# Performance work log

Measured on AMD Instinct MI355X. Metric: run time of the kernel, lower is better.

## Reference

```python
import jax, jax.numpy as jnp
import numpy as np

NB_STEPS = 50
ALPHA = 0.9
NUM_RNN_STEPS = 2
B = 4096
NUM_FEATURE = 100
IN_D = 5
HIDDEN = [64, 64, 64]
P1 = (1.1, 1.1, 1.5, 2.0, 2.5)   # IntegrandNN_outer_level powers
P2 = (1.5, 2.0, 2.5, 3.0, 3.5)   # IntegrandNN powers


def _cc(nb_steps):
    # Clenshaw-Curtis weights/steps, identical to UMNN's compute_cc_weights
    n = nb_steps
    i = np.arange(n + 1, dtype=np.float64).reshape(-1, 1)
    lam = np.cos(i @ i.T * np.pi / n)
    lam[:, 0] = 0.5
    lam[:, -1] *= 0.5
    lam = lam * 2.0 / n
    W = np.zeros(n + 1)
    even = np.arange(0, n + 1, 2)
    W[even] = 2.0 / (1.0 - even.astype(np.float64) ** 2)
    W[0] = 1.0
    ccw = (lam.T @ W).astype(np.float32)                         # [n+1]
    steps = np.cos(np.arange(n + 1) * np.pi / n).astype(np.float32)  # [n+1]
    return jnp.asarray(ccw), jnp.asarray(steps)

CC_W, CC_S = _cc(NB_STEPS)


def _mlp(xh, Ws, bs):
    # Linear+ReLU stack with ELU on the last layer (ReLU popped, ELU appended)
    h = xh
    for W, b in zip(Ws[:-1], bs[:-1]):
        h = jax.nn.relu(h @ W.T + b)
    return jax.nn.elu(h @ Ws[-1].T + bs[-1])


def _integrand(x, h, Ws, bs, Wf, powers):
    z = _mlp(jnp.concatenate([x, h], axis=1), Ws, bs) + 1.0      # [N,1], z >= 0
    feats = jnp.concatenate([z ** p for p in powers], axis=1)    # [N,5]
    return jax.nn.relu((1.0 / (feats + 1.0)) @ Wf.T)             # [N,1]


def _integrate(x0, xT, h, f):
    # ParallelNeuralIntegral forward: CC quadrature of f from x0 to xT
    Bn, S = x0.shape[0], NB_STEPS + 1
    X = x0[:, None, :] + (xT - x0)[:, None, :] * (CC_S[None, :, None] + 1.0) / 2.0  # [B,S,1]
    hs = jnp.broadcast_to(h[:, None, :], (Bn, S, h.shape[1])).reshape(-1, h.shape[1])
    dz = f(X.reshape(-1, 1), hs).reshape(Bn, S, 1)
    return (dz * CC_W[None, :, None]).sum(1) * (xT - x0) / 2.0   # [B,1]


def setup_inputs() -> dict:
    key = jax.random.key(0)
    ks = jax.random.split(key, 24)
    def lin(k, o, i):
        return jax.random.normal(k, (o, i), jnp.float32) / np.sqrt(i)
    d = {}
    d["x_"] = jax.random.normal(ks[0], (B, NUM_FEATURE), jnp.float32)
    d["h_"] = jax.random.normal(ks[1], (B, IN_D - 1), jnp.float32)
    d["log_weight"] = jnp.ones((1, NUM_FEATURE), jnp.float32)     # reset_parameters -> 1
    d["sigmoid_param"] = jnp.zeros((1,), jnp.float32)
    sizes = [IN_D] + HIDDEN + [1]
    for tag, base in (("f1", 2), ("f2", 12)):
        for li, (i, o) in enumerate(zip(sizes[:-1], sizes[1:])):
            d[f"{tag}_W{li}"] = lin(ks[base + 2 * li], o, i)
            d[f"{tag}_b{li}"] = jnp.zeros((o,), jnp.float32)
        d[f"{tag}_Wf"] = jnp.abs(lin(ks[base + 9], 1, 5))         # reset_params -> abs
    return d


def reference(x_, h_, log_weight, sigmoid_param,
              f1_W0, f1_b0, f1_W1, f1_b1, f1_W2, f1_b2, f1_W3, f1_b3, f1_Wf,
              f2_W0, f2_b0, f2_W1, f2_b1, f2_W2, f2_b2, f2_W3, f2_b3, f2_Wf):
    f1Ws = [f1_W0, f1_W1, f1_W2, f1_W3]; f1bs = [f1_b0, f1_b1, f1_b2, f1_b3]
    f2Ws = [f2_W0, f2_W1, f2_W2, f2_W3]; f2bs = [f2_b0, f2_b1, f2_b2, f2_b3]
    f1 = lambda x, h: _integrand(x, h, f1Ws, f1bs, f1_Wf, P1)
    f2 = lambda x, h: _integrand(x, h, f2Ws, f2bs, f2_Wf, P2)

    # modular function: linear to [B,1] then sum over dim 1 -> [B,1]
    xm = jnp.sum(x_ * log_weight[0], axis=1, keepdims=True)
    lam = jax.nn.sigmoid(sigmoid_param[0])

    I1 = jnp.zeros_like(xm)
    I2 = jnp.zeros_like(xm)
    out_first = None
    for _ in range(NUM_RNN_STEPS):
        x = (1.0 - lam) * xm + lam * I1
        x2 = (1.0 - lam) * xm + lam * I2
        out_first = f1(x2, h_)
        I1 = _integrate(jnp.zeros_like(x), x, h_, f1)
        xmax = jnp.max(x2) + 10.0
        xfinal = jnp.zeros_like(x) + xmax
        I2 = (1.0 / ALPHA) * _integrate(x2, xfinal, h_, f2)
    return I1, out_first, I2
```

## Files before the change

kernel.cpp:

```cpp
#include <hip/hip_runtime.h>
#include <math.h>

typedef _Float16 half8v __attribute__((ext_vector_type(8)));
typedef _Float16 half4v __attribute__((ext_vector_type(4)));
typedef _Float16 half2v __attribute__((ext_vector_type(2)));
typedef float float4v __attribute__((ext_vector_type(4)));

#define BB    4096
#define INV_ALPHA (1.0f/0.9f)

#define WS_CCW  0
#define WS_CCS  64
#define WS_LAM  128
#define WS_PM   256
#define WS_XM   512
#define WS_A1   4608
#define WS_A2   8704
#define WS_H    16384
#define H_NET   8192
#define H_W2    4096
#define H_W0    16384
#define H_W3    20480

#if defined(__has_builtin)
#if __has_builtin(__builtin_amdgcn_rcpf)
#define FRCP(x) __builtin_amdgcn_rcpf(x)
#endif
#if __has_builtin(__builtin_amdgcn_exp2f)
#define FEXP2(x) __builtin_amdgcn_exp2f(x)
#endif
#if __has_builtin(__builtin_amdgcn_logf)
#define FLOG2(x) __builtin_amdgcn_logf(x)
#endif
#endif
#ifndef FRCP
#define FRCP(x) (1.0f / (x))
#endif
#ifndef FEXP2
#define FEXP2(x) exp2f(x)
#endif
#ifndef FLOG2
#define FLOG2(x) log2f(x)
#endif

__device__ __forceinline__ int swz(int row, int cb) {
    return (row << 6) + (((cb ^ (row & 7)) & 7) << 3);
}

__device__ __forceinline__ half4v pk_relu4(float4v c) {
#if defined(__has_builtin) && __has_builtin(__builtin_amdgcn_cvt_pkrtz)
    half2v a = __builtin_bit_cast(half2v,
        __builtin_amdgcn_cvt_pkrtz(fmaxf(c[0], 0.0f), fmaxf(c[1], 0.0f)));
    half2v b = __builtin_bit_cast(half2v,
        __builtin_amdgcn_cvt_pkrtz(fmaxf(c[2], 0.0f), fmaxf(c[3], 0.0f)));
    half4v o; o[0] = a[0]; o[1] = a[1]; o[2] = b[0]; o[3] = b[1];
    return o;
#else
    half4v o;
    o[0] = (_Float16)fmaxf(c[0], 0.0f); o[1] = (_Float16)fmaxf(c[1], 0.0f);
    o[2] = (_Float16)fmaxf(c[2], 0.0f); o[3] = (_Float16)fmaxf(c[3], 0.0f);
    return o;
#endif
}

__device__ __forceinline__ float tail5(float y,
        float p0, float p1, float p2, float p3, float p4,
        float wf0, float wf1, float wf2, float wf3, float wf4) {
    if (y <= 0.0f) y = FEXP2(y * 1.44269504f) - 1.0f;
    float z = y + 1.0f;
    float lg = FLOG2(z);
    float g = wf0 * FRCP(FEXP2(p0 * lg) + 1.0f)
            + wf1 * FRCP(FEXP2(p1 * lg) + 1.0f)
            + wf2 * FRCP(FEXP2(p2 * lg) + 1.0f)
            + wf3 * FRCP(FEXP2(p3 * lg) + 1.0f)
            + wf4 * FRCP(FEXP2(p4 * lg) + 1.0f);
    return fmaxf(g, 0.0f);
}

__global__ void k_setup(const float* __restrict__ x_, const float* __restrict__ lw,
                        const float* __restrict__ sp,
                        const float* __restrict__ f1W0, const float* __restrict__ f1W1,
                        const float* __restrict__ f1W2, const float* __restrict__ f1W3,
                        const float* __restrict__ f2W0, const float* __restrict__ f2W1,
                        const float* __restrict__ f2W2, const float* __restrict__ f2W3,
                        float* __restrict__ ws, float* __restrict__ out) {
    _Float16* wh = (_Float16*)(ws + WS_H);
    const int blk = blockIdx.x, tid = threadIdx.x;
    if (blk < 256) {
        int wave = tid >> 6, lane = tid & 63;
        float vmax = -1e30f;
        for (int r = 0; r < 4; ++r) {
            int row = blk * 16 + wave * 4 + r;
            float v = 0.0f;
            for (int i = lane; i < 100; i += 64) v = fmaf(x_[row * 100 + i], lw[i], v);
            #pragma unroll
            for (int off = 32; off > 0; off >>= 1) v += __shfl_xor(v, off, 64);
            if (lane == 0) ws[WS_XM + row] = v;
            vmax = fmaxf(vmax, v);
        }
        __shared__ float sm[4];
        if (lane == 0) sm[wave] = vmax;
        __syncthreads();
        if (tid == 0)
            ws[WS_PM + blk] = fmaxf(fmaxf(sm[0], sm[1]), fmaxf(sm[2], sm[3]));
    } else if (blk < 272) {
        int t = (blk - 256) * 256 + tid;
        wh[t]                = (_Float16)f1W1[t];
        wh[H_W2 + t]         = (_Float16)f1W2[t];
        wh[H_NET + t]        = (_Float16)f2W1[t];
        wh[H_NET + H_W2 + t] = (_Float16)f2W2[t];
        if (t < 2048) {
            int j = t >> 5, k = t & 31;
            wh[H_W0 + t]        = (k < 5) ? (_Float16)f1W0[j * 5 + k] : (_Float16)0.0f;
            wh[H_W0 + 2048 + t] = (k < 5) ? (_Float16)f2W0[j * 5 + k] : (_Float16)0.0f;
        }
        if (t < 64) {
            wh[H_W3 + t]      = (_Float16)f1W3[t];
            wh[H_W3 + 64 + t] = (_Float16)f2W3[t];
        }
    } else if (blk == 272) {
        if (tid == 64) ws[WS_LAM] = 1.0f / (1.0f + expf(-sp[0]));
        if (tid <= 50) {
            int s = tid;
            ws[WS_CCS + s] = cospif((float)s / 50.0f);
            float acc = 0.0f;
            for (int a = 0; a <= 50; ++a) {
                float w;
                if (a == 0) w = 1.0f;
                else if ((a & 1) == 0) w = 2.0f / (1.0f - (float)(a * a));
                else continue;
                float l;
                if (s == 0) l = 0.5f;
                else {
                    int m = (a * s) % 100;
                    l = cospif((float)m / 50.0f);
                    if (s == 50) l *= 0.5f;
                }
                acc += l * 0.04f * w;
            }
            ws[WS_CCW + s] = acc;
        }
    } else if (blk < 305) {
        int t = (blk - 273) * 256 + tid;
        out[t < BB ? t : BB + t] = 0.0f;
    } else {
        int t = (blk - 305) * 256 + tid;
        ws[WS_A1 + t] = 0.0f;
    }
}

__global__ __launch_bounds__(256, 2) void k_int(
    int mode, float* __restrict__ ws, const float* __restrict__ h_,
    const float* __restrict__ f1b0, const float* __restrict__ f1b1,
    const float* __restrict__ f1b2, const float* __restrict__ f1b3,
    const float* __restrict__ f1Wf,
    const float* __restrict__ f2b0, const float* __restrict__ f2b1,
    const float* __restrict__ f2b2, const float* __restrict__ f2b3,
    const float* __restrict__ f2Wf,
    float* __restrict__ out)
{
    __shared__ _Float16 act[4 * 64 * 64];
    __shared__ _Float16 w0f[4 * 16 * 8];
    __shared__ _Float16 w1f[512 * 8];
    __shared__ _Float16 w2f[512 * 8];
    __shared__ float bl[192];

    const int tid = threadIdx.x;
    const int blk = blockIdx.x;
    const int wloc = tid >> 6;
    const int lane = tid & 63;
    const int lo = lane & 15, q = lane >> 4;

    const int g = blk >> 2;
    const int w = (blk & 3) * 4 + wloc;
    const bool u2 = (g >= 64);
    const int base = (g & 63) << 6;
    const bool of_wave = (mode != 0) && (!u2) && (w == 15);

    const float* xm = ws + WS_XM;
    const float* a1p = ws + WS_A1;
    const float* a2p = ws + WS_A2;
    const _Float16* wh = (const _Float16*)(ws + WS_H);
    const float lam = ws[WS_LAM];
    const float oml = 1.0f - lam;

    const _Float16* W0h = wh + H_W0 + (u2 ? 2048 : 0);
    const _Float16* W1h = wh + (u2 ? H_NET : 0);
    const _Float16* W2h = W1h + H_W2;
    const _Float16* W3h = wh + H_W3 + (u2 ? 64 : 0);
    const float* B0 = u2 ? f2b0 : f1b0;
    const float* B1 = u2 ? f2b1 : f1b1;
    const float* B2 = u2 ? f2b2 : f1b2;
    const float* B3 = u2 ? f2b3 : f1b3;
    const float* WF = u2 ? f2Wf : f1Wf;
    const float p0 = u2 ? 1.5f : 1.1f;
    const float p1 = u2 ? 2.0f : 1.1f;
    const float p2 = u2 ? 2.5f : 1.5f;
    const float p3 = u2 ? 3.0f : 2.0f;
    const float p4 = u2 ? 3.5f : 2.5f;

    #pragma unroll
    for (int f = tid; f < 512; f += 256) {
        int fm = f >> 7, fkb = (f >> 6) & 1, fl = f & 63;
        int flo = fl & 15, fq = fl >> 4;
        *(half8v*)(w1f + f * 8) =
            *(const half8v*)(W1h + (16 * fm + flo) * 64 + fkb * 32 + fq * 8);
        *(half8v*)(w2f + f * 8) =
            *(const half8v*)(W2h + (16 * fm + flo) * 64 + fkb * 32 + fq * 8);
    }
    if (tid < 64) {
        int fm = tid >> 4, flo = tid & 15;
        *(half8v*)(w0f + tid * 8) = *(const half8v*)(W0h + (16 * fm + flo) * 32);
    }
    if (tid < 192)
        bl[tid] = (tid < 64) ? B0[tid] : (tid < 128) ? B1[tid - 64] : B2[tid - 128];

    half4v w3r[4];
    #pragma unroll
    for (int m = 0; m < 4; ++m)
        w3r[m] = *(const half4v*)(W3h + 16 * m + 4 * q);
    const float B3s = B3[0];
    const float wf0 = WF[0], wf1 = WF[1], wf2 = WF[2], wf3 = WF[3], wf4 = WF[4];

    half8v zf;
    #pragma unroll
    for (int t2 = 0; t2 < 8; ++t2) zf[t2] = (_Float16)0.0f;

    float xr_r[4], x2_r[4];
    half8v tpl[4];
    #pragma unroll
    for (int n = 0; n < 4; ++n) {
        int idx = base + 16 * n + lo;
        float xmv = xm[idx];
        if (mode == 0) {
            xr_r[n] = oml * xmv;
        } else {
            float a = u2 ? a2p[idx] : a1p[idx];
            xr_r[n] = fmaf(lam, a, oml * xmv);
        }
        float4 h4 = ((const float4*)h_)[idx];
        half8v e = zf;
        e[1] = (_Float16)h4.x; e[2] = (_Float16)h4.y;
        e[3] = (_Float16)h4.z; e[4] = (_Float16)h4.w;
        tpl[n] = (q == 0) ? e : zf;
        x2_r[n] = 0.0f;
    }
    if (of_wave) {
        #pragma unroll
        for (int n = 0; n < 4; ++n) {
            int idx = base + 16 * n + lo;
            x2_r[n] = fmaf(lam, a2p[idx], oml * xm[idx]);
        }
    }

    float xmax = 0.0f;
    if (u2) {
        if (mode) {
            float v = -1e30f;
            #pragma unroll 4
            for (int j = 0; j < 16; ++j) {
                int i = j * 256 + lane * 4;
                float4 xm4 = *(const float4*)(xm + i);
                float4 a24 = *(const float4*)(a2p + i);
                v = fmaxf(v, fmaf(lam, a24.x, oml * xm4.x));
                v = fmaxf(v, fmaf(lam, a24.y, oml * xm4.y));
                v = fmaxf(v, fmaf(lam, a24.z, oml * xm4.z));
                v = fmaxf(v, fmaf(lam, a24.w, oml * xm4.w));
            }
            #pragma unroll
            for (int off = 32; off > 0; off >>= 1) v = fmaxf(v, __shfl_xor(v, off, 64));
            xmax = v + 10.0f;
        } else {
            const float* pm = ws + WS_PM;
            float v = fmaxf(fmaxf(pm[lane], pm[lane + 64]),
                            fmaxf(pm[lane + 128], pm[lane + 192]));
            #pragma unroll
            for (int off = 32; off > 0; off >>= 1) v = fmaxf(v, __shfl_xor(v, off, 64));
            xmax = oml * v + 10.0f;
        }
    }

    __syncthreads();

    _Float16* actw = act + (wloc << 12);
    const int np = (w < 3 || of_wave) ? 4 : 3;
    float acc = 0.0f;

    #pragma clang loop unroll(disable)
    for (int p = 0; p < np; ++p) {
        const bool of_iter = of_wave && (p == 3);
        float t = 0.0f, ccw_s = 0.0f;
        if (!of_iter) {
            int s = w + 16 * p;
            t = (ws[WS_CCS + s] + 1.0f) * 0.5f;
            ccw_s = ws[WS_CCW + s];
        }

        half8v Bf0[4];
        #pragma unroll
        for (int n = 0; n < 4; ++n) {
            float xin;
            if (of_iter) xin = x2_r[n];
            else if (u2) xin = fmaf(t, xmax - xr_r[n], xr_r[n]);
            else         xin = xr_r[n] * t;
            half8v b = tpl[n];
            b[0] = (_Float16)((q == 0) ? xin : 0.0f);
            Bf0[n] = b;
        }

        #pragma unroll
        for (int m = 0; m < 4; ++m) {
            half8v a0 = (q == 0) ? *(const half8v*)(w0f + (m * 16 + lo) * 8) : zf;
            float4v b0 = *(const float4v*)(bl + 16 * m + 4 * q);
            #pragma unroll
            for (int n = 0; n < 4; ++n) {
                float4v c = __builtin_amdgcn_mfma_f32_16x16x32_f16(a0, Bf0[n], b0, 0, 0, 0);
                *(half4v*)(actw + swz(16 * n + lo, 2 * m + (q >> 1)) + 4 * (q & 1)) = pk_relu4(c);
            }
        }

        {
            half8v Bf[2][4];
            #pragma unroll
            for (int kb = 0; kb < 2; ++kb)
                #pragma unroll
                for (int n = 0; n < 4; ++n)
                    Bf[kb][n] = *(const half8v*)(actw + swz(16 * n + lo, 4 * kb + q));
            #pragma unroll
            for (int m = 0; m < 4; ++m) {
                half8v a10 = *(const half8v*)(w1f + ((m * 2 + 0) * 64 + lane) * 8);
                half8v a11 = *(const half8v*)(w1f + ((m * 2 + 1) * 64 + lane) * 8);
                float4v b1 = *(const float4v*)(bl + 64 + 16 * m + 4 * q);
                #pragma unroll
                for (int n = 0; n < 4; ++n) {
                    float4v c = __builtin_amdgcn_mfma_f32_16x16x32_f16(a10, Bf[0][n], b1, 0, 0, 0);
                    c = __builtin_amdgcn_mfma_f32_16x16x32_f16(a11, Bf[1][n], c, 0, 0, 0);
                    *(half4v*)(actw + swz(16 * n + lo, 2 * m + (q >> 1)) + 4 * (q & 1)) = pk_relu4(c);
                }
            }
        }

        float part[4] = {0.0f, 0.0f, 0.0f, 0.0f};
        {
            half8v Bf[2][4];
            #pragma unroll
            for (int kb = 0; kb < 2; ++kb)
                #pragma unroll
                for (int n = 0; n < 4; ++n)
                    Bf[kb][n] = *(const half8v*)(actw + swz(16 * n + lo, 4 * kb + q));
            #pragma unroll
            for (int m = 0; m < 4; ++m) {
                half8v a20 = *(const half8v*)(w2f + ((m * 2 + 0) * 64 + lane) * 8);
                half8v a21 = *(const half8v*)(w2f + ((m * 2 + 1) * 64 + lane) * 8);
                float4v b2 = *(const float4v*)(bl + 128 + 16 * m + 4 * q);
                #pragma unroll
                for (int n = 0; n < 4; ++n) {
                    float4v c = __builtin_amdgcn_mfma_f32_16x16x32_f16(a20, Bf[0][n], b2, 0, 0, 0);
                    c = __builtin_amdgcn_mfma_f32_16x16x32_f16(a21, Bf[1][n], c, 0, 0, 0);
                    #pragma unroll
                    for (int e = 0; e < 4; ++e)
                        part[n] = fmaf((float)w3r[m][e], fmaxf(c[e], 0.0f), part[n]);
                }
            }
        }

        #pragma unroll
        for (int n = 0; n < 4; ++n) {
            part[n] += __shfl_xor(part[n], 16, 64);
            part[n] += __shfl_xor(part[n], 32, 64);
        }
        float y = B3s + (q == 0 ? part[0] : q == 1 ? part[1] : q == 2 ? part[2] : part[3]);

        float val = tail5(y, p0, p1, p2, p3, p4, wf0, wf1, wf2, wf3, wf4);

        if (of_iter) out[BB + base + lane] = val;
        else         acc = fmaf(ccw_s, val, acc);
    }

    const float x_l = (q == 0 ? xr_r[0] : q == 1 ? xr_r[1] : q == 2 ? xr_r[2] : xr_r[3]);
    if (mode == 0) {
        if (!u2) atomicAdd(ws + WS_A1 + base + lane, acc * x_l * 0.5f);
        else     atomicAdd(ws + WS_A2 + base + lane, acc * (xmax - x_l) * 0.5f * INV_ALPHA);
    } else {
        if (!u2) atomicAdd(out + base + lane, acc * x_l * 0.5f);
        else     atomicAdd(out + 2 * BB + base + lane,
                           acc * (xmax - x_l) * 0.5f * INV_ALPHA);
    }
}

extern "C" void kernel_launch(void* const* d_in, const int* in_sizes, int n_in,
                              void* d_out, int out_size, void* d_ws, size_t ws_size,
                              hipStream_t stream) {
    const float* x_  = (const float*)d_in[0];
    const float* h_  = (const float*)d_in[1];
    const float* lw  = (const float*)d_in[2];
    const float* sp  = (const float*)d_in[3];
    const float* f1W0 = (const float*)d_in[4];   const float* f1b0 = (const float*)d_in[5];
    const float* f1W1 = (const float*)d_in[6];   const float* f1b1 = (const float*)d_in[7];
    const float* f1W2 = (const float*)d_in[8];   const float* f1b2 = (const float*)d_in[9];
    const float* f1W3 = (const float*)d_in[10];  const float* f1b3 = (const float*)d_in[11];
    const float* f1Wf = (const float*)d_in[12];
    const float* f2W0 = (const float*)d_in[13];  const float* f2b0 = (const float*)d_in[14];
    const float* f2W1 = (const float*)d_in[15];  const float* f2b1 = (const float*)d_in[16];
    const float* f2W2 = (const float*)d_in[17];  const float* f2b2 = (const float*)d_in[18];
    const float* f2W3 = (const float*)d_in[19];  const float* f2b3 = (const float*)d_in[20];
    const float* f2Wf = (const float*)d_in[21];
    float* out = (float*)d_out;
    float* ws  = (float*)d_ws;

    k_setup<<<337, 256, 0, stream>>>(x_, lw, sp,
                                     f1W0, f1W1, f1W2, f1W3,
                                     f2W0, f2W1, f2W2, f2W3, ws, out);
    k_int<<<512, 256, 0, stream>>>(0, ws, h_,
        f1b0, f1b1, f1b2, f1b3, f1Wf, f2b0, f2b1, f2b2, f2b3, f2Wf, out);
    k_int<<<512, 256, 0, stream>>>(1, ws, h_,
        f1b0, f1b1, f1b2, f1b3, f1Wf, f2b0, f2b1, f2b2, f2b3, f2Wf, out);
}
```

Baseline: 138.3 us.

## Interleave two quadrature steps per wave and use 512-thread blocks

Result: slower. 180.2 us (+30.3%).

```diff
diff --git a/kernel.cpp b/kernel.cpp
--- a/kernel.cpp
+++ b/kernel.cpp
@@ -149,7 +149,7 @@
     }
 }
 
-__global__ __launch_bounds__(256, 2) void k_int(
+__global__ __launch_bounds__(512, 2) void k_int(
     int mode, float* __restrict__ ws, const float* __restrict__ h_,
     const float* __restrict__ f1b0, const float* __restrict__ f1b1,
     const float* __restrict__ f1b2, const float* __restrict__ f1b3,
@@ -159,7 +159,7 @@
     const float* __restrict__ f2Wf,
     float* __restrict__ out)
 {
-    __shared__ _Float16 act[4 * 64 * 64];
+    __shared__ _Float16 act[8 * 2 * 64 * 64];
     __shared__ _Float16 w0f[4 * 16 * 8];
     __shared__ _Float16 w1f[512 * 8];
     __shared__ _Float16 w2f[512 * 8];
@@ -171,8 +171,8 @@
     const int lane = tid & 63;
     const int lo = lane & 15, q = lane >> 4;
 
-    const int g = blk >> 2;
-    const int w = (blk & 3) * 4 + wloc;
+    const int g = blk >> 1;
+    const int w = (blk & 1) * 8 + wloc;
     const bool u2 = (g >= 64);
     const int base = (g & 63) << 6;
     const bool of_wave = (mode != 0) && (!u2) && (w == 15);
@@ -199,8 +199,8 @@
     const float p3 = u2 ? 3.0f : 2.0f;
     const float p4 = u2 ? 3.5f : 2.5f;
 
-    #pragma unroll
-    for (int f = tid; f < 512; f += 256) {
+    if (tid < 512) {
+        int f = tid;
         int fm = f >> 7, fkb = (f >> 6) & 1, fl = f & 63;
         int flo = fl & 15, fq = fl >> 4;
         *(half8v*)(w1f + f * 8) =
@@ -282,50 +282,58 @@
 
     __syncthreads();
 
-    _Float16* actw = act + (wloc << 12);
-    const int np = (w < 3 || of_wave) ? 4 : 3;
+    _Float16* actw = act + (wloc << 13);
     float acc = 0.0f;
 
     #pragma clang loop unroll(disable)
-    for (int p = 0; p < np; ++p) {
-        const bool of_iter = of_wave && (p == 3);
-        float t = 0.0f, ccw_s = 0.0f;
-        if (!of_iter) {
-            int s = w + 16 * p;
-            t = (ws[WS_CCS + s] + 1.0f) * 0.5f;
-            ccw_s = ws[WS_CCW + s];
-        }
-
-        half8v Bf0[4];
+    for (int dp = 0; dp < 2; ++dp) {
+        const int s0 = w + 32 * dp;
+        const bool live1 = (dp == 0) || (w < 3);
+        const int s1 = live1 ? (s0 + 16) : s0;
+        const bool of1 = of_wave && (dp == 1);
+        const float t0 = (ws[WS_CCS + s0] + 1.0f) * 0.5f;
+        const float cw0 = ws[WS_CCW + s0];
+        const float t1 = (ws[WS_CCS + s1] + 1.0f) * 0.5f;
+        const float cw1 = live1 ? ws[WS_CCW + s1] : 0.0f;
+
+        {
+            half8v Bf0[2][4];
+            #pragma unroll
+            for (int j = 0; j < 2; ++j) {
+                const float tj = j ? t1 : t0;
+                #pragma unroll
+                for (int n = 0; n < 4; ++n) {
+                    float xin;
+                    if (j == 1 && of1) xin = x2_r[n];
+                    else if (u2)       xin = fmaf(tj, xmax - xr_r[n], xr_r[n]);
+                    else               xin = xr_r[n] * tj;
+                    half8v b = tpl[n];
+                    b[0] = (_Float16)((q == 0) ? xin : 0.0f);
+                    Bf0[j][n] = b;
+                }
+            }
+            #pragma unroll
+            for (int m = 0; m < 4; ++m) {
+                half8v a0 = (q == 0) ? *(const half8v*)(w0f + (m * 16 + lo) * 8) : zf;
+                float4v b0 = *(const float4v*)(bl + 16 * m + 4 * q);
+                #pragma unroll
+                for (int j = 0; j < 2; ++j)
+                    #pragma unroll
+                    for (int n = 0; n < 4; ++n) {
+                        float4v c = __builtin_amdgcn_mfma_f32_16x16x32_f16(a0, Bf0[j][n], b0, 0, 0, 0);
+                        *(half4v*)(actw + (j << 12) + swz(16 * n + lo, 2 * m + (q >> 1)) + 4 * (q & 1)) = pk_relu4(c);
+                    }
+            }
+        }
+
         #pragma unroll
-        for (int n = 0; n < 4; ++n) {
-            float xin;
-            if (of_iter) xin = x2_r[n];
-            else if (u2) xin = fmaf(t, xmax - xr_r[n], xr_r[n]);
-            else         xin = xr_r[n] * t;
-            half8v b = tpl[n];
-            b[0] = (_Float16)((q == 0) ? xin : 0.0f);
-            Bf0[n] = b;
-        }
-
-        #pragma unroll
-        for (int m = 0; m < 4; ++m) {
-            half8v a0 = (q == 0) ? *(const half8v*)(w0f + (m * 16 + lo) * 8) : zf;
-            float4v b0 = *(const float4v*)(bl + 16 * m + 4 * q);
-            #pragma unroll
-            for (int n = 0; n < 4; ++n) {
-                float4v c = __builtin_amdgcn_mfma_f32_16x16x32_f16(a0, Bf0[n], b0, 0, 0, 0);
-                *(half4v*)(actw + swz(16 * n + lo, 2 * m + (q >> 1)) + 4 * (q & 1)) = pk_relu4(c);
-            }
-        }
-
-        {
+        for (int j = 0; j < 2; ++j) {
             half8v Bf[2][4];
             #pragma unroll
             for (int kb = 0; kb < 2; ++kb)
                 #pragma unroll
                 for (int n = 0; n < 4; ++n)
-                    Bf[kb][n] = *(const half8v*)(actw + swz(16 * n + lo, 4 * kb + q));
+                    Bf[kb][n] = *(const half8v*)(actw + (j << 12) + swz(16 * n + lo, 4 * kb + q));
             #pragma unroll
             for (int m = 0; m < 4; ++m) {
                 half8v a10 = *(const half8v*)(w1f + ((m * 2 + 0) * 64 + lane) * 8);
@@ -335,19 +343,20 @@
                 for (int n = 0; n < 4; ++n) {
                     float4v c = __builtin_amdgcn_mfma_f32_16x16x32_f16(a10, Bf[0][n], b1, 0, 0, 0);
                     c = __builtin_amdgcn_mfma_f32_16x16x32_f16(a11, Bf[1][n], c, 0, 0, 0);
-                    *(half4v*)(actw + swz(16 * n + lo, 2 * m + (q >> 1)) + 4 * (q & 1)) = pk_relu4(c);
+                    *(half4v*)(actw + (j << 12) + swz(16 * n + lo, 2 * m + (q >> 1)) + 4 * (q & 1)) = pk_relu4(c);
                 }
             }
         }
 
-        float part[4] = {0.0f, 0.0f, 0.0f, 0.0f};
-        {
+        float part[2][4] = {{0.0f, 0.0f, 0.0f, 0.0f}, {0.0f, 0.0f, 0.0f, 0.0f}};
+        #pragma unroll
+        for (int j = 0; j < 2; ++j) {
             half8v Bf[2][4];
             #pragma unroll
             for (int kb = 0; kb < 2; ++kb)
                 #pragma unroll
                 for (int n = 0; n < 4; ++n)
-                    Bf[kb][n] = *(const half8v*)(actw + swz(16 * n + lo, 4 * kb + q));
+                    Bf[kb][n] = *(const half8v*)(actw + (j << 12) + swz(16 * n + lo, 4 * kb + q));
             #pragma unroll
             for (int m = 0; m < 4; ++m) {
                 half8v a20 = *(const half8v*)(w2f + ((m * 2 + 0) * 64 + lane) * 8);
@@ -359,22 +368,27 @@
                     c = __builtin_amdgcn_mfma_f32_16x16x32_f16(a21, Bf[1][n], c, 0, 0, 0);
                     #pragma unroll
                     for (int e = 0; e < 4; ++e)
-                        part[n] = fmaf((float)w3r[m][e], fmaxf(c[e], 0.0f), part[n]);
+                        part[j][n] = fmaf((float)w3r[m][e], fmaxf(c[e], 0.0f), part[j][n]);
                 }
             }
         }
 
         #pragma unroll
-        for (int n = 0; n < 4; ++n) {
-            part[n] += __shfl_xor(part[n], 16, 64);
-            part[n] += __shfl_xor(part[n], 32, 64);
-        }
-        float y = B3s + (q == 0 ? part[0] : q == 1 ? part[1] : q == 2 ? part[2] : part[3]);
-
-        float val = tail5(y, p0, p1, p2, p3, p4, wf0, wf1, wf2, wf3, wf4);
-
-        if (of_iter) out[BB + base + lane] = val;
-        else         acc = fmaf(ccw_s, val, acc);
+        for (int j = 0; j < 2; ++j)
+            #pragma unroll
+            for (int n = 0; n < 4; ++n) {
+                part[j][n] += __shfl_xor(part[j][n], 16, 64);
+                part[j][n] += __shfl_xor(part[j][n], 32, 64);
+            }
+        float y0 = B3s + (q == 0 ? part[0][0] : q == 1 ? part[0][1] : q == 2 ? part[0][2] : part[0][3]);
+        float y1 = B3s + (q == 0 ? part[1][0] : q == 1 ? part[1][1] : q == 2 ? part[1][2] : part[1][3]);
+
+        float val0 = tail5(y0, p0, p1, p2, p3, p4, wf0, wf1, wf2, wf3, wf4);
+        float val1 = tail5(y1, p0, p1, p2, p3, p4, wf0, wf1, wf2, wf3, wf4);
+
+        acc = fmaf(cw0, val0, acc);
+        acc = fmaf(cw1, val1, acc);
+        if (of1) out[BB + base + lane] = val1;
     }
 
     const float x_l = (q == 0 ? xr_r[0] : q == 1 ? xr_r[1] : q == 2 ? xr_r[2] : xr_r[3]);
@@ -411,8 +425,8 @@
     k_setup<<<337, 256, 0, stream>>>(x_, lw, sp,
                                      f1W0, f1W1, f1W2, f1W3,
                                      f2W0, f2W1, f2W2, f2W3, ws, out);
-    k_int<<<512, 256, 0, stream>>>(0, ws, h_,
+    k_int<<<256, 512, 0, stream>>>(0, ws, h_,
         f1b0, f1b1, f1b2, f1b3, f1Wf, f2b0, f2b1, f2b2, f2b3, f2Wf, out);
-    k_int<<<512, 256, 0, stream>>>(1, ws, h_,
+    k_int<<<256, 512, 0, stream>>>(1, ws, h_,
         f1b0, f1b1, f1b2, f1b3, f1Wf, f2b0, f2b1, f2b2, f2b3, f2Wf, out);
 }
```
